# Kernel tuning notes

Hardware: AMD Instinct MI355X
Metric: run time of the kernel (lower is better)

The kernel has to match this reference:

```python
import jax, jax.numpy as jnp
import numpy as np

H = 64          # hidden_size / SINDy latent dim
DM = 128        # d_model (GRU input size)
FF = 128        # dim_feedforward
NL = 2          # num_sindy_layers
EPS = 1e-5      # LayerNorm eps (torch default)
TRI_I, TRI_J = np.triu_indices(H)          # poly_order=2 pairs, torch loop order (i<=j)
LIB = 1 + H + TRI_I.size                   # 2145


def layernorm(x, g, b):
    m = jnp.mean(x, axis=-1, keepdims=True)
    v = jnp.mean((x - m) ** 2, axis=-1, keepdims=True)
    return (x - m) * jax.lax.rsqrt(v + EPS) * g + b


def sindy_library(z):
    # z: (N, H) -> Theta: (N, 1 + H + H*(H+1)/2); same term ordering as torch loops
    ones = jnp.ones((z.shape[0], 1), z.dtype)
    quad = z[:, TRI_I] * z[:, TRI_J]
    return jnp.concatenate([ones, z, quad], axis=1)


def gru_layer(x, Wih, Whh, bih, bhh):
    # x: (B, S, in), Wih: (3H, in), Whh: (3H, H); torch GRU gate order r,z,n
    xp = jnp.einsum('bsi,gi->bsg', x, Wih) + bih  # (B,S,3H) precomputed input projections
    B = x.shape[0]

    def step(h, xpt):
        gh = h @ Whh.T + bhh
        r = jax.nn.sigmoid(xpt[:, :H] + gh[:, :H])
        z = jax.nn.sigmoid(xpt[:, H:2 * H] + gh[:, H:2 * H])
        n = jnp.tanh(xpt[:, 2 * H:] + r * gh[:, 2 * H:])
        h = (1.0 - z) * n + z * h
        return h, h

    h0 = jnp.zeros((B, H), x.dtype)
    _, ys = jax.lax.scan(step, h0, jnp.swapaxes(xp, 0, 1))  # scan over time
    return jnp.swapaxes(ys, 0, 1)  # (B, S, H)


def sindy_layer(src, coef, g1, b1n, W1, bf1, W2, bf2, g2, b2n):
    B, S, _ = src.shape
    theta = sindy_library(src.reshape(-1, H))          # (N, LIB)
    upd = (theta @ coef).reshape(B, S, H)              # (B, S, H)
    src = layernorm(src + upd, g1, b1n)                # dropout = identity (eval)
    ff = jax.nn.gelu(src @ W1.T + bf1, approximate=False) @ W2.T + bf2
    return layernorm(src + ff, g2, b2n)


def setup_inputs() -> dict:
    key = jax.random.key(0)
    ks = jax.random.split(key, 24)
    f = lambda k, sh, s=0.05: (jax.random.normal(k, sh, dtype=jnp.float32) * s)
    inp = {
        'x': jax.random.normal(ks[0], (32, 500, DM), dtype=jnp.float32),
        # GRU layer 0 (input DM) and layer 1 (input H)
        'Wih0': f(ks[1], (3 * H, DM)), 'Whh0': f(ks[2], (3 * H, H)),
        'bih0': f(ks[3], (3 * H,)), 'bhh0': f(ks[4], (3 * H,)),
        'Wih1': f(ks[5], (3 * H, H)), 'Whh1': f(ks[6], (3 * H, H)),
        'bih1': f(ks[7], (3 * H,)), 'bhh1': f(ks[8], (3 * H,)),
        # stacked params for NL=2 identical SINDy layers
        'coeffs': f(ks[9], (NL, LIB, H), 0.02),
        'ln1_g': jnp.ones((NL, H), jnp.float32), 'ln1_b': jnp.zeros((NL, H), jnp.float32),
        'W1': f(ks[10], (NL, FF, H)), 'b1': f(ks[11], (NL, FF)),
        'W2': f(ks[12], (NL, H, FF)), 'b2': f(ks[13], (NL, H)),
        'ln2_g': jnp.ones((NL, H), jnp.float32), 'ln2_b': jnp.zeros((NL, H), jnp.float32),
    }
    return inp


def reference(x, Wih0, Whh0, bih0, bhh0, Wih1, Whh1, bih1, bhh1,
              coeffs, ln1_g, ln1_b, W1, b1, W2, b2, ln2_g, ln2_b):
    h = gru_layer(x, Wih0, Whh0, bih0, bhh0)
    h = gru_layer(h, Wih1, Whh1, bih1, bhh1)
    for l in range(NL):
        h = sindy_layer(h, coeffs[l], ln1_g[l], ln1_b[l], W1[l], b1[l],
                        W2[l], b2[l], ln2_g[l], ln2_b[l])
    return h, h[:, -1, :]
```

## Files before the change

### kernel.cpp

```cpp
#include <hip/hip_runtime.h>
#include <hip/hip_bf16.h>
#include <math.h>

#define H 64
#define DM 128
#define GDIM 192
#define BSZ 32
#define SEQ 500
#define NROW (BSZ*SEQ)
#define LIBN 2145
#define FFD 128
#define NKC2 75
#define NGRP 300
#define CPK2 153600

typedef __attribute__((ext_vector_type(8))) short short8;
typedef __attribute__((ext_vector_type(4))) float f32x4;
typedef __attribute__((ext_vector_type(2))) float f32x2;
typedef __attribute__((ext_vector_type(4))) unsigned u32x4;

__device__ __forceinline__ float sigf(float x) {
    return 1.0f / (1.0f + __expf(-x));
}
__device__ __forceinline__ float tanhfast(float x) {
    x = fminf(fmaxf(x, -15.0f), 15.0f);
    float t = __expf(-2.0f * x);
    return (1.0f - t) / (1.0f + t);
}
__device__ __forceinline__ short bf16r(float f) {
    unsigned u = __float_as_uint(f);
    unsigned r = (u + 0x7fffu + ((u >> 16) & 1u)) >> 16;
    return (short)r;
}
__device__ __forceinline__ f32x2 pkfma(f32x2 a, f32x2 b, f32x2 c) {
    f32x2 d;
    asm("v_pk_fma_f32 %0, %1, %2, %3" : "=v"(d) : "v"(a), "v"(b), "v"(c));
    return d;
}

__device__ __forceinline__ void grp_decode(int g, int& a, int& b) {
    if (g < 8) { a = 64; b = g * 8; }
    else if (g == 8 || g >= 297) { a = 64; b = 64; }
    else {
        int G = g - 9, acc = 0;
        a = 0; b = 0;
        for (int i2 = 0; i2 < 64; i2++) {
            int cnt = 8 - (i2 >> 3);
            if (G < acc + cnt) { a = i2; b = ((i2 >> 3) + (G - acc)) * 8; break; }
            acc += cnt;
        }
    }
}

__global__ void pack_all(const float* __restrict__ wih0,
                         const float* __restrict__ coeffs,
                         const float* __restrict__ w1,
                         const float* __restrict__ w2,
                         float* __restrict__ wtp,
                         short* __restrict__ bfa) {
    int idx = blockIdx.x * 256 + threadIdx.x;
    if (idx < GDIM * DM) {
        int e  = idx & 3;
        int g  = (idx >> 2) % GDIM;
        int k4 = idx / (GDIM * 4);
        wtp[idx] = wih0[g * DM + k4 * 4 + e];
        return;
    }
    int r = idx - GDIM * DM;
    int l = r / (CPK2 + 2 * 8192);
    int q = r % (CPK2 + 2 * 8192);
    if (q < CPK2) {
        const float* coef = coeffs + (size_t)l * LIBN * H;
        int j = q & 7, lane = (q >> 3) & 63, nt = (q >> 9) & 3, kc = q >> 11;
        int grp = kc * 4 + (lane >> 4);
        int row = -1;
        if (grp < 8) row = 1 + grp * 8 + j;
        else if (grp == 8) row = (j == 0) ? 0 : -1;
        else if (grp < 297) {
            int a, b;
            grp_decode(grp, a, b);
            int jdx = b + j;
            if (jdx >= a) row = 65 + a * 64 - (a * (a - 1)) / 2 + (jdx - a);
        }
        int c = nt * 16 + (lane & 15);
        bfa[(size_t)l * CPK2 + q] = (row >= 0) ? bf16r(coef[(size_t)row * H + c]) : (short)0;
        return;
    }
    int q2 = q - CPK2;
    if (q2 < 8192) {
        const float* w1l = w1 + (size_t)l * FFD * H;
        int j = q2 & 7, lane = (q2 >> 3) & 63, nt = (q2 >> 9) & 7, kc = q2 >> 12;
        int k = kc * 32 + ((lane >> 4) << 3) + j;
        int n = nt * 16 + (lane & 15);
        bfa[(size_t)2 * CPK2 + l * 8192 + q2] = bf16r(w1l[(size_t)n * H + k]);
        return;
    }
    int q3 = q2 - 8192;
    const float* w2l = w2 + (size_t)l * H * FFD;
    int j = q3 & 7, lane = (q3 >> 3) & 63, nt = (q3 >> 9) & 3, kc = q3 >> 11;
    int k = kc * 32 + ((lane >> 4) << 3) + j;
    int n = nt * 16 + (lane & 15);
    bfa[(size_t)2 * CPK2 + 2 * 8192 + l * 8192 + q3] = bf16r(w2l[(size_t)n * FFD + k]);
}

__global__ __launch_bounds__(192, 2) void xp0_gemm(const float* __restrict__ x,
                                                   const float* __restrict__ wtp,
                                                   const float* __restrict__ bih0,
                                                   float* __restrict__ xpT) {
    __shared__ float xs[64][DM];
    int rb = blockIdx.x * 64;
    for (int idx = threadIdx.x; idx < 64 * 32; idx += 192) {
        int r = idx >> 5, k4 = idx & 31;
        ((f32x4*)xs[r])[k4] = ((const f32x4*)(x + (size_t)(rb + r) * DM))[k4];
    }
    __syncthreads();
    int g = threadIdx.x;
    float bias = bih0[g];
    float acc[64];
#pragma unroll
    for (int r = 0; r < 64; r++) acc[r] = bias;
    for (int k4 = 0; k4 < 32; k4++) {
        f32x4 w4 = ((const f32x4*)wtp)[k4 * GDIM + g];
#pragma unroll
        for (int r = 0; r < 64; r++) {
            f32x4 xv = ((f32x4*)xs[r])[k4];
            acc[r] += w4[0] * xv[0] + w4[1] * xv[1] + w4[2] * xv[2] + w4[3] * xv[3];
        }
    }
    for (int r = 0; r < 64; r++) {
        int row = rb + r;
        int bb = row / 500;
        int ss = row - bb * 500;
        xpT[(((size_t)bb * 125 + (ss >> 2)) * GDIM + g) * 4 + (ss & 3)] = acc[r];
    }
}

__global__ __launch_bounds__(768, 3) void gru_fused(const float* __restrict__ xpT,
                                                    const float* __restrict__ whh0,
                                                    const float* __restrict__ bhh0,
                                                    const float* __restrict__ wih1,
                                                    const float* __restrict__ bih1,
                                                    const float* __restrict__ whh1,
                                                    const float* __restrict__ bhh1,
                                                    float* __restrict__ hbuf) {
    int b = blockIdx.x;
    int tid = threadIdx.x;
    int wv = __builtin_amdgcn_readfirstlane(tid >> 6);
    int lane = tid & 63;
    int m = wv % 3;
    int q = wv / 3;
    int k0 = q * 16;

    __shared__ __align__(16) float h0s[H];
    __shared__ __align__(16) float h1s[H];
    __shared__ float part[3][4][GDIM];

    if (tid < H) { h0s[tid] = 0.0f; h1s[tid] = 0.0f; }

    const float* W = (m == 0) ? whh0 : (m == 1) ? wih1 : whh1;
    f32x2 wrp[8], wzp[8], wnp[8];
#pragma unroll
    for (int k4 = 0; k4 < 4; k4++) {
        f32x4 a = ((const f32x4*)(W + (size_t)lane * H + k0))[k4];
        f32x4 c = ((const f32x4*)(W + (size_t)(H + lane) * H + k0))[k4];
        f32x4 d = ((const f32x4*)(W + (size_t)(2 * H + lane) * H + k0))[k4];
        wrp[2*k4]   = __builtin_shufflevector(a, a, 0, 1);
        wrp[2*k4+1] = __builtin_shufflevector(a, a, 2, 3);
        wzp[2*k4]   = __builtin_shufflevector(c, c, 0, 1);
        wzp[2*k4+1] = __builtin_shufflevector(c, c, 2, 3);
        wnp[2*k4]   = __builtin_shufflevector(d, d, 0, 1);
        wnp[2*k4+1] = __builtin_shufflevector(d, d, 2, 3);
    }

    float b0r = 0, b0z = 0, b0n = 0;
    float b1ir = 0, b1iz = 0, b1in = 0, b1hr = 0, b1hz = 0, b1hn = 0;
    float hreg0 = 0.0f, hreg1 = 0.0f;
    float hb4[4] = {0.f, 0.f, 0.f, 0.f};
    f32x4 xc[4][3];
    const float* xpB = xpT + (size_t)b * 125 * GDIM * 4;

    if (wv == 0) {
        b0r = bhh0[lane]; b0z = bhh0[H + lane]; b0n = bhh0[2 * H + lane];
#pragma unroll
        for (int g3 = 0; g3 < 3; g3++) {
            xc[0][g3] = *(const f32x4*)(xpB + ((size_t)0 * GDIM + g3 * 64 + lane) * 4);
            xc[1][g3] = *(const f32x4*)(xpB + ((size_t)1 * GDIM + g3 * 64 + lane) * 4);
        }
    } else if (wv == 2) {
        b1ir = bih1[lane]; b1iz = bih1[H + lane]; b1in = bih1[2 * H + lane];
        b1hr = bhh1[lane]; b1hz = bhh1[H + lane]; b1hn = bhh1[2 * H + lane];
    }
    __syncthreads();

    auto loadch = [&](int c, int buf) {
        if (c < 125) {
#pragma unroll
            for (int g3 = 0; g3 < 3; g3++)
                xc[buf][g3] = *(const f32x4*)(xpB + ((size_t)c * GDIM + g3 * 64 + lane) * 4);
        }
    };

    auto step = [&](int s, int e, float xr, float xz, float xn) {
        const float* hv = (m == 2) ? h1s : h0s;
        f32x2 arp = {0.f, 0.f}, azp = {0.f, 0.f}, anp = {0.f, 0.f};
#pragma unroll
        for (int t4 = 0; t4 < 4; t4++) {
            f32x4 h4 = ((const f32x4*)(hv + k0))[t4];
            f32x2 hlo = __builtin_shufflevector(h4, h4, 0, 1);
            f32x2 hhi = __builtin_shufflevector(h4, h4, 2, 3);
            arp = pkfma(wrp[2*t4], hlo, arp);
            arp = pkfma(wrp[2*t4+1], hhi, arp);
            azp = pkfma(wzp[2*t4], hlo, azp);
            azp = pkfma(wzp[2*t4+1], hhi, azp);
            anp = pkfma(wnp[2*t4], hlo, anp);
            anp = pkfma(wnp[2*t4+1], hhi, anp);
        }
        part[m][q][lane] = arp[0] + arp[1];
        part[m][q][H + lane] = azp[0] + azp[1];
        part[m][q][2 * H + lane] = anp[0] + anp[1];
        __syncthreads();

        if (wv == 0) {
            if (s < SEQ) {
                float gr = b0r, gz = b0z, gn = b0n;
#pragma unroll
                for (int qq = 0; qq < 4; qq++) {
                    gr += part[0][qq][lane];
                    gz += part[0][qq][H + lane];
                    gn += part[0][qq][2 * H + lane];
                }
                float rg = sigf(xr + gr);
                float zg = sigf(xz + gz);
                float ng = tanhfast(xn + rg * gn);
                hreg0 = (1.0f - zg) * ng + zg * hreg0;
                h0s[lane] = hreg0;
            }
        } else if (wv == 2) {
            if (s >= 1) {
                float xr1 = b1ir, xz1 = b1iz, xn1 = b1in;
                float gr1 = b1hr, gz1 = b1hz, gn1 = b1hn;
#pragma unroll
                for (int qq = 0; qq < 4; qq++) {
                    xr1 += part[1][qq][lane];
                    xz1 += part[1][qq][H + lane];
                    xn1 += part[1][qq][2 * H + lane];
                    gr1 += part[2][qq][lane];
                    gz1 += part[2][qq][H + lane];
                    gn1 += part[2][qq][2 * H + lane];
                }
                float rg = sigf(xr1 + gr1);
                float zg = sigf(xz1 + gz1);
                float ng = tanhfast(xn1 + rg * gn1);
                hreg1 = (1.0f - zg) * ng + zg * hreg1;
                h1s[lane] = hreg1;
                hb4[(e + 3) & 3] = hreg1;
                if (e == 0) {
                    float* dst = hbuf + ((size_t)b * SEQ + (s - 4)) * H + lane;
#pragma unroll
                    for (int t = 0; t < 4; t++) dst[t * H] = hb4[t];
                }
            }
        }
        __syncthreads();
    };

    for (int scb = 0; scb < 31; scb++) {
#pragma unroll
        for (int sci = 0; sci < 4; sci++) {
            int sc = scb * 4 + sci;
            if (wv == 0 && (sci & 1) == 0) {
                loadch(sc + 2, (sci + 2) & 3);
                loadch(sc + 3, (sci + 3) & 3);
            }
            int s0 = sc * 4;
            step(s0 + 0, 0, xc[sci][0][0], xc[sci][1][0], xc[sci][2][0]);
            step(s0 + 1, 1, xc[sci][0][1], xc[sci][1][1], xc[sci][2][1]);
            step(s0 + 2, 2, xc[sci][0][2], xc[sci][1][2], xc[sci][2][2]);
            step(s0 + 3, 3, xc[sci][0][3], xc[sci][1][3], xc[sci][2][3]);
        }
    }
    {
        step(496, 0, xc[0][0][0], xc[0][1][0], xc[0][2][0]);
        step(497, 1, xc[0][0][1], xc[0][1][1], xc[0][2][1]);
        step(498, 2, xc[0][0][2], xc[0][1][2], xc[0][2][2]);
        step(499, 3, xc[0][0][3], xc[0][1][3], xc[0][2][3]);
    }
    step(500, 0, 0.0f, 0.0f, 0.0f);
}

__global__ __launch_bounds__(512) void sindy_fused(const float* __restrict__ hbuf_in,
                                                   const short* __restrict__ bfa,
                                                   const float* __restrict__ ln1g,
                                                   const float* __restrict__ ln1b,
                                                   const float* __restrict__ b1g,
                                                   const float* __restrict__ b2g,
                                                   const float* __restrict__ ln2g,
                                                   const float* __restrict__ ln2b,
                                                   float* __restrict__ out) {
    __shared__ float z[65 * 68];
    __shared__ float upd[64 * 68];
    __shared__ float ff[64 * 132];
    __shared__ unsigned kmap2[NGRP];
    __shared__ float bfs1[2][FFD], bfs2[2][H];
    __shared__ float g1s[2][H], b1s[2][H], g2s[2][H], b2s[2][H];

    int tid = threadIdx.x;
    int wv = __builtin_amdgcn_readfirstlane(tid >> 6);
    int lane = tid & 63;
    int row0 = blockIdx.x * 64;

    for (int idx = tid; idx < 64 * 16; idx += 512) {
        int r = idx >> 4, c4 = idx & 15;
        *(f32x4*)&z[r * 68 + c4 * 4] = *(const f32x4*)&hbuf_in[(size_t)(row0 + r) * H + c4 * 4];
    }
    for (int idx = tid; idx < 64 * 17; idx += 512)
        *(f32x4*)&upd[idx * 4] = (f32x4){0.f, 0.f, 0.f, 0.f};
    if (tid < 64) {
        z[tid * 68 + 64] = 1.0f; z[tid * 68 + 65] = 0.0f;
        z[tid * 68 + 66] = 0.0f; z[tid * 68 + 67] = 0.0f;
    }
    if (tid < 68) z[64 * 68 + tid] = 0.0f;
    if (tid < NGRP) {
        int a, b;
        grp_decode(tid, a, b);
        kmap2[tid] = ((unsigned)a << 16) | (unsigned)b;
    }
    if (tid < FFD) { bfs1[0][tid] = b1g[tid]; bfs1[1][tid] = b1g[FFD + tid]; }
    if (tid < H) {
        bfs2[0][tid] = b2g[tid];      bfs2[1][tid] = b2g[H + tid];
        g1s[0][tid] = ln1g[tid];      g1s[1][tid] = ln1g[H + tid];
        b1s[0][tid] = ln1b[tid];      b1s[1][tid] = ln1b[H + tid];
        g2s[0][tid] = ln2g[tid];      g2s[1][tid] = ln2g[H + tid];
        b2s[0][tid] = ln2b[tid];      b2s[1][tid] = ln2b[H + tid];
    }
    __syncthreads();

    int kj0 = ((lane >> 4) << 3);
    int m0 = (wv & 3) * 16;
    int m = m0 + (lane & 15);
    int rbase = m0 + ((lane >> 4) << 2);
    int cb16 = lane & 15;
    const float* zrow = &z[m * 68];
    int lrow = tid >> 3;
    int lk = (tid & 7) * 8;

#pragma unroll
    for (int l = 0; l < 2; l++) {
        const short* cpk = bfa + (size_t)l * CPK2;
        const short* w1p = bfa + (size_t)2 * CPK2 + l * 8192;
        const short* w2p = bfa + (size_t)2 * CPK2 + 2 * 8192 + l * 8192;

        {
            int p = wv >> 2;
            f32x4 acc[4] = {{0,0,0,0},{0,0,0,0},{0,0,0,0},{0,0,0,0}};
            for (int kc = p; kc < NKC2; kc += 2) {
                unsigned ab = kmap2[kc * 4 + (lane >> 4)];
                float za = zrow[ab >> 16];
                const float* zb = &zrow[ab & 0xffffu];
                f32x4 z0 = *(const f32x4*)zb;
                f32x4 z1 = *(const f32x4*)(zb + 4);
                short8 af;
                af[0] = bf16r(za * z0[0]);
                af[1] = bf16r(za * z0[1]);
                af[2] = bf16r(za * z0[2]);
                af[3] = bf16r(za * z0[3]);
                af[4] = bf16r(za * z1[0]);
                af[5] = bf16r(za * z1[1]);
                af[6] = bf16r(za * z1[2]);
                af[7] = bf16r(za * z1[3]);
                const short* cb = cpk + ((size_t)(kc * 4) * 64 + lane) * 8;
#pragma unroll
                for (int nt = 0; nt < 4; nt++) {
                    short8 bf = *(const short8*)(cb + (size_t)nt * 512);
                    acc[nt] = __builtin_amdgcn_mfma_f32_16x16x32_bf16(af, bf, acc[nt], 0, 0, 0);
                }
            }
#pragma unroll
            for (int nt = 0; nt < 4; nt++)
#pragma unroll
                for (int r = 0; r < 4; r++)
                    atomicAdd(&upd[(rbase + r) * 68 + nt * 16 + cb16], acc[nt][r]);
        }
        __syncthreads();

        {
            float v[8];
            float s1 = 0.0f;
#pragma unroll
            for (int i = 0; i < 8; i++) {
                v[i] = z[lrow * 68 + lk + i] + upd[lrow * 68 + lk + i];
                s1 += v[i];
            }
            s1 += __shfl_xor(s1, 1); s1 += __shfl_xor(s1, 2); s1 += __shfl_xor(s1, 4);
            float mn = s1 * (1.0f / 64.0f);
            float s2 = 0.0f;
#pragma unroll
            for (int i = 0; i < 8; i++) { float d = v[i] - mn; s2 += d * d; }
            s2 += __shfl_xor(s2, 1); s2 += __shfl_xor(s2, 2); s2 += __shfl_xor(s2, 4);
            float rstd = 1.0f / sqrtf(s2 * (1.0f / 64.0f) + 1e-5f);
#pragma unroll
            for (int i = 0; i < 8; i++)
                z[lrow * 68 + lk + i] = (v[i] - mn) * rstd * g1s[l][lk + i] + b1s[l][lk + i];
        }
        __syncthreads();

        {
            int nq = wv >> 2;
            f32x4 acc[4] = {{0,0,0,0},{0,0,0,0},{0,0,0,0},{0,0,0,0}};
#pragma unroll
            for (int kc = 0; kc < 2; kc++) {
                f32x4 za = *(const f32x4*)&z[m * 68 + kc * 32 + kj0];
                f32x4 zb = *(const f32x4*)&z[m * 68 + kc * 32 + kj0 + 4];
                short8 af;
                af[0] = bf16r(za[0]); af[1] = bf16r(za[1]); af[2] = bf16r(za[2]); af[3] = bf16r(za[3]);
                af[4] = bf16r(zb[0]); af[5] = bf16r(zb[1]); af[6] = bf16r(zb[2]); af[7] = bf16r(zb[3]);
#pragma unroll
                for (int t = 0; t < 4; t++) {
                    int nt = nq * 4 + t;
                    short8 bf = *(const short8*)(w1p + ((size_t)(kc * 8 + nt) * 64 + lane) * 8);
                    acc[t] = __builtin_amdgcn_mfma_f32_16x16x32_bf16(af, bf, acc[t], 0, 0, 0);
                }
            }
#pragma unroll
            for (int t = 0; t < 4; t++) {
                int col = (nq * 4 + t) * 16 + cb16;
#pragma unroll
                for (int r = 0; r < 4; r++) {
                    float v = acc[t][r] + bfs1[l][col];
                    ff[(rbase + r) * 132 + col] = 0.5f * v * (1.0f + erff(v * 0.70710678118654752f));
                }
            }
        }
        __syncthreads();

        {
            int nh = wv >> 2;
            f32x4 acc[2] = {{0,0,0,0},{0,0,0,0}};
            const float* frow = &ff[m * 132];
#pragma unroll
            for (int kc = 0; kc < 4; kc++) {
                f32x4 fa = *(const f32x4*)&frow[kc * 32 + kj0];
                f32x4 fb = *(const f32x4*)&frow[kc * 32 + kj0 + 4];
                short8 af;
                af[0] = bf16r(fa[0]); af[1] = bf16r(fa[1]); af[2] = bf16r(fa[2]); af[3] = bf16r(fa[3]);
                af[4] = bf16r(fb[0]); af[5] = bf16r(fb[1]); af[6] = bf16r(fb[2]); af[7] = bf16r(fb[3]);
#pragma unroll
                for (int t = 0; t < 2; t++) {
                    int nt = nh * 2 + t;
                    short8 bf = *(const short8*)(w2p + ((size_t)(kc * 4 + nt) * 64 + lane) * 8);
                    acc[t] = __builtin_amdgcn_mfma_f32_16x16x32_bf16(af, bf, acc[t], 0, 0, 0);
                }
            }
#pragma unroll
            for (int t = 0; t < 2; t++) {
                int col = (nh * 2 + t) * 16 + cb16;
#pragma unroll
                for (int r = 0; r < 4; r++)
                    upd[(rbase + r) * 68 + col] = acc[t][r] + bfs2[l][col];
            }
        }
        __syncthreads();

        {
            float v[8];
            float s1 = 0.0f;
#pragma unroll
            for (int i = 0; i < 8; i++) {
                v[i] = z[lrow * 68 + lk + i] + upd[lrow * 68 + lk + i];
                s1 += v[i];
            }
            s1 += __shfl_xor(s1, 1); s1 += __shfl_xor(s1, 2); s1 += __shfl_xor(s1, 4);
            float mn = s1 * (1.0f / 64.0f);
            float s2 = 0.0f;
#pragma unroll
            for (int i = 0; i < 8; i++) { float d = v[i] - mn; s2 += d * d; }
            s2 += __shfl_xor(s2, 1); s2 += __shfl_xor(s2, 2); s2 += __shfl_xor(s2, 4);
            float rstd = 1.0f / sqrtf(s2 * (1.0f / 64.0f) + 1e-5f);
            if (l == 0) {
#pragma unroll
                for (int i = 0; i < 8; i++)
                    z[lrow * 68 + lk + i] = (v[i] - mn) * rstd * g2s[0][lk + i] + b2s[0][lk + i];
            } else {
                int row = row0 + lrow;
                int last = (row % SEQ == SEQ - 1);
#pragma unroll
                for (int i = 0; i < 8; i++) {
                    float res = (v[i] - mn) * rstd * g2s[1][lk + i] + b2s[1][lk + i];
                    out[(size_t)row * H + lk + i] = res;
                    if (last)
                        out[(size_t)NROW * H + (row / SEQ) * H + lk + i] = res;
                }
            }
        }
        __syncthreads();

        if (l == 0) {
            for (int idx = tid; idx < 64 * 17; idx += 512)
                *(f32x4*)&upd[idx * 4] = (f32x4){0.f, 0.f, 0.f, 0.f};
            __syncthreads();
        }
    }
}

extern "C" void kernel_launch(void* const* d_in, const int* in_sizes, int n_in,
                              void* d_out, int out_size, void* d_ws, size_t ws_size,
                              hipStream_t stream) {
    const float* x    = (const float*)d_in[0];
    const float* wih0 = (const float*)d_in[1];
    const float* whh0 = (const float*)d_in[2];
    const float* bih0 = (const float*)d_in[3];
    const float* bhh0 = (const float*)d_in[4];
    const float* wih1 = (const float*)d_in[5];
    const float* whh1 = (const float*)d_in[6];
    const float* bih1 = (const float*)d_in[7];
    const float* bhh1 = (const float*)d_in[8];
    const float* coeffs = (const float*)d_in[9];
    const float* ln1g = (const float*)d_in[10];
    const float* ln1b = (const float*)d_in[11];
    const float* w1   = (const float*)d_in[12];
    const float* b1   = (const float*)d_in[13];
    const float* w2   = (const float*)d_in[14];
    const float* b2   = (const float*)d_in[15];
    const float* ln2g = (const float*)d_in[16];
    const float* ln2b = (const float*)d_in[17];

    float* out = (float*)d_out;
    float* ws  = (float*)d_ws;
    float* xpT = ws;
    float* wtp = ws + (size_t)NROW * GDIM;
    short* bfa = (short*)(wtp + GDIM * DM);
    float* hbuf = out;

    pack_all<<<1424, 256, 0, stream>>>(wih0, coeffs, w1, w2, wtp, bfa);
    xp0_gemm<<<NROW / 64, 192, 0, stream>>>(x, wtp, bih0, xpT);
    gru_fused<<<BSZ, 768, 0, stream>>>(xpT, whh0, bhh0, wih1, bih1, whh1, bhh1, hbuf);
    sindy_fused<<<NROW / 64, 512, 0, stream>>>(hbuf, bfa, ln1g, ln1b, b1, b2,
                                               ln2g, ln2b, out);
}
```

Baseline: 510.2 us.

## Restructure input-projection GEMM with LDS-resident weights and 4x4 register tiles

The input-projection GEMM for GRU layer 0 now stages the whole transposed Wih0 matrix (96 KB) in LDS and gives each thread a 4-row by 12-column register tile. Previously it staged the 64 x rows in LDS and kept 64 accumulators per thread. The weight pack is simplified to a plain k-major transpose to match. The aim is more reuse per load and vectorized 16-byte stores into the time-blocked xpT layout. The 96 KB of LDS limits occupancy to about one block per CU, and every block reloads the full weight matrix.

```diff
diff --git a/kernel.cpp b/kernel.cpp
--- a/kernel.cpp
+++ b/kernel.cpp
@@ -60,10 +60,9 @@
                          short* __restrict__ bfa) {
     int idx = blockIdx.x * 256 + threadIdx.x;
     if (idx < GDIM * DM) {
-        int e  = idx & 3;
-        int g  = (idx >> 2) % GDIM;
-        int k4 = idx / (GDIM * 4);
-        wtp[idx] = wih0[g * DM + k4 * 4 + e];
+        int k = idx / GDIM;
+        int g = idx - k * GDIM;
+        wtp[idx] = wih0[g * DM + k];
         return;
     }
     int r = idx - GDIM * DM;
@@ -103,35 +102,62 @@
     bfa[(size_t)2 * CPK2 + 2 * 8192 + l * 8192 + q3] = bf16r(w2l[(size_t)n * FFD + k]);
 }
 
-__global__ __launch_bounds__(192, 2) void xp0_gemm(const float* __restrict__ x,
-                                                   const float* __restrict__ wtp,
+__global__ __launch_bounds__(256, 1) void xp0_gemm(const float* __restrict__ x,
+                                                   const float* __restrict__ wt2,
                                                    const float* __restrict__ bih0,
                                                    float* __restrict__ xpT) {
-    __shared__ float xs[64][DM];
+    __shared__ __align__(16) float wlds[DM * GDIM];
+    int tid = threadIdx.x;
+    int wv = __builtin_amdgcn_readfirstlane(tid >> 6);
+    int lane = tid & 63;
+
+    for (int p = tid; p < DM * GDIM / 4; p += 256)
+        ((f32x4*)wlds)[p] = ((const f32x4*)wt2)[p];
+
+    int i = lane >> 2;
+    int j = lane & 3;
     int rb = blockIdx.x * 64;
-    for (int idx = threadIdx.x; idx < 64 * 32; idx += 192) {
-        int r = idx >> 5, k4 = idx & 31;
-        ((f32x4*)xs[r])[k4] = ((const f32x4*)(x + (size_t)(rb + r) * DM))[k4];
+    int row0 = rb + 4 * i;
+
+    f32x4 acc[3][4];
+#pragma unroll
+    for (int t = 0; t < 3; t++) {
+        f32x4 bv = *(const f32x4*)(bih0 + 16 * (wv + 4 * t) + 4 * j);
+#pragma unroll
+        for (int ii = 0; ii < 4; ii++) acc[t][ii] = bv;
     }
     __syncthreads();
-    int g = threadIdx.x;
-    float bias = bih0[g];
-    float acc[64];
-#pragma unroll
-    for (int r = 0; r < 64; r++) acc[r] = bias;
+
+    const float* xr0 = x + (size_t)row0 * DM;
     for (int k4 = 0; k4 < 32; k4++) {
-        f32x4 w4 = ((const f32x4*)wtp)[k4 * GDIM + g];
-#pragma unroll
-        for (int r = 0; r < 64; r++) {
-            f32x4 xv = ((f32x4*)xs[r])[k4];
-            acc[r] += w4[0] * xv[0] + w4[1] * xv[1] + w4[2] * xv[2] + w4[3] * xv[3];
-        }
-    }
-    for (int r = 0; r < 64; r++) {
-        int row = rb + r;
-        int bb = row / 500;
-        int ss = row - bb * 500;
-        xpT[(((size_t)bb * 125 + (ss >> 2)) * GDIM + g) * 4 + (ss & 3)] = acc[r];
+        f32x4 xr[4];
+#pragma unroll
+        for (int ii = 0; ii < 4; ii++)
+            xr[ii] = *(const f32x4*)(xr0 + ii * DM + k4 * 4);
+#pragma unroll
+        for (int t = 0; t < 3; t++) {
+            int cb = 16 * (wv + 4 * t);
+#pragma unroll
+            for (int e = 0; e < 4; e++) {
+                f32x4 wvv = *(const f32x4*)&wlds[(k4 * 4 + e) * GDIM + cb + 4 * j];
+#pragma unroll
+                for (int ii = 0; ii < 4; ii++)
+                    acc[t][ii] += wvv * xr[ii][e];
+            }
+        }
+    }
+    int bb = row0 / 500;
+    int ss = row0 - bb * 500;
+    float* base = xpT + ((size_t)(bb * 125 + (ss >> 2)) * GDIM) * 4;
+#pragma unroll
+    for (int t = 0; t < 3; t++) {
+        int cb = 16 * (wv + 4 * t);
+#pragma unroll
+        for (int jj = 0; jj < 4; jj++) {
+            int g = cb + 4 * j + jj;
+            f32x4 v = { acc[t][0][jj], acc[t][1][jj], acc[t][2][jj], acc[t][3][jj] };
+            *(f32x4*)(base + (size_t)g * 4) = v;
+        }
     }
 }
 
@@ -532,7 +558,7 @@
     float* hbuf = out;
 
     pack_all<<<1424, 256, 0, stream>>>(wih0, coeffs, w1, w2, wtp, bfa);
-    xp0_gemm<<<NROW / 64, 192, 0, stream>>>(x, wtp, bih0, xpT);
+    xp0_gemm<<<NROW / 64, 256, 0, stream>>>(x, wtp, bih0, xpT);
     gru_fused<<<BSZ, 768, 0, stream>>>(xpT, whh0, bhh0, wih1, bih1, whh1, bhh1, hbuf);
     sindy_fused<<<NROW / 64, 512, 0, stream>>>(hbuf, bfa, ln1g, ln1b, b1, b2,
                                                ln2g, ln2b, out);
```

Measured after the change: 465.8 us, median of 2. -8.7%, faster.
